# Optimization experiments

Measured on AMD Instinct MI355X. Metric: run time of the kernel, lower is better.

Reference implementation:

```python
import jax, jax.numpy as jnp
from jax import lax
import numpy as np

H = 64
IN = 32
OUT = 32


def _rnn_layer(x, Wih, Whh, bih, bhh):
    # x: [B,T,I]; PyTorch RNN: h_t = tanh(x_t Wih^T + bih + h_{t-1} Whh^T + bhh)
    B = x.shape[0]
    xW = jnp.einsum('bti,hi->bth', x, Wih) + (bih + bhh)  # fuse biases

    def step(h, xw_t):
        h_new = jnp.tanh(xw_t + h @ Whh.T)
        return h_new, h_new

    h0 = jnp.zeros((B, Whh.shape[0]), x.dtype)
    hT, outs = lax.scan(step, h0, jnp.swapaxes(xW, 0, 1))  # scan over T
    return jnp.swapaxes(outs, 0, 1), hT  # [B,T,H], [B,H]


def setup_inputs() -> dict:
    key = jax.random.key(0)
    ks = jax.random.split(key, 12)
    s1 = 1.0 / np.sqrt(H)
    u = lambda k, shape: jax.random.uniform(k, shape, jnp.float32, -s1, s1)
    return {
        'x': jax.random.normal(ks[0], (1024, 512, IN), jnp.float32),
        'Wih1': u(ks[1], (H, IN)), 'Whh1': u(ks[2], (H, H)),
        'bih1': u(ks[3], (H,)), 'bhh1': u(ks[4], (H,)),
        'Wih2': u(ks[5], (H, H)), 'Whh2': u(ks[6], (H, H)),
        'bih2': u(ks[7], (H,)), 'bhh2': u(ks[8], (H,)),
        'W_fc1': u(ks[9], (H, H)), 'b_fc1': u(ks[9], (H,)),
        'W_fc2': u(ks[10], (OUT, H)), 'b_fc2': u(ks[11], (OUT,)),
    }


def reference(x, Wih1, Whh1, bih1, bhh1, Wih2, Whh2, bih2, bhh2,
              W_fc1, b_fc1, W_fc2, b_fc2):
    out1, _ = _rnn_layer(x, Wih1, Whh1, bih1, bhh1)
    _, h2 = _rnn_layer(out1, Wih2, Whh2, bih2, bhh2)
    z = jax.nn.relu(h2 @ W_fc1.T + b_fc1)
    return z @ W_fc2.T + b_fc2  # [B,32]
```

## Files before the change

### kernel.cpp

```cpp
#include <hip/hip_runtime.h>
#include <stdint.h>

#define HH 64
#define II 32
#define TSTEPS 512
#define BATCH 1024
#define CH2 32
#define NCH2 (TSTEPS / CH2)
#define XWBYTES ((size_t)BATCH * TSTEPS * HH * 4)

typedef float f32x2 __attribute__((ext_vector_type(2)));
typedef float f32x4 __attribute__((ext_vector_type(4)));

__device__ __forceinline__ float fast_tanh(float x) {
    float e = __builtin_amdgcn_exp2f(x * 2.885390081777927f);
    return fmaf(-2.0f, __builtin_amdgcn_rcpf(e + 1.0f), 1.0f);
}

#define LOADW2(dst, src, N)                                                   \
    {                                                                         \
        const f32x4* p_ = (const f32x4*)(src);                                \
        _Pragma("unroll") for (int k_ = 0; k_ < (N) / 4; ++k_) {              \
            f32x4 v_ = p_[k_];                                                \
            dst[2 * k_] = v_.lo;                                              \
            dst[2 * k_ + 1] = v_.hi;                                          \
        }                                                                     \
    }

__global__ void __launch_bounds__(256) xw_precompute(
    const float* __restrict__ x,
    const float* __restrict__ Wih1,
    const float* __restrict__ bih1,
    const float* __restrict__ bhh1,
    float* __restrict__ xw)
{
    const int tid = threadIdx.x;
    const int w = tid >> 6;
    const int l = tid & 63;
    const int rbase = blockIdx.x * 64;

    __shared__ __align__(16) float xsm[64 * II];

    const float* gx = x + (size_t)rbase * II;
#pragma unroll
    for (int k = 0; k < 2; ++k) {
        const int off = w * 512 + k * 256;
        __builtin_amdgcn_global_load_lds(
            (const __attribute__((address_space(1))) void*)(gx + off + l * 4),
            (__attribute__((address_space(3))) void*)(xsm + off),
            16, 0, 0);
    }
    asm volatile("s_waitcnt vmcnt(0)" ::: "memory");
    __syncthreads();

    f32x2 wv[II / 2];
    LOADW2(wv, Wih1 + l * II, II);
    const float bb = bih1[l] + bhh1[l];
    float* outb = xw + (size_t)rbase * HH;

#pragma unroll
    for (int i = 0; i < 16; ++i) {
        const int r = w + i * 4;
        const float* xr = xsm + r * II;
        f32x2 a0 = {bb, 0.f}, a1 = {0.f, 0.f};
#pragma unroll
        for (int k = 0; k < II / 4; ++k) {
            f32x4 q = *(const f32x4*)(xr + 4 * k);
            a0 = __builtin_elementwise_fma(q.lo, wv[2 * k], a0);
            a1 = __builtin_elementwise_fma(q.hi, wv[2 * k + 1], a1);
        }
        outb[r * HH + l] = (a0.x + a1.x) + (a0.y + a1.y);
    }
}

__global__ void __launch_bounds__(128, 2) rnn_rec(
    const float* __restrict__ xw,
    const float* __restrict__ Whh1,
    const float* __restrict__ Wih2,
    const float* __restrict__ Whh2,
    const float* __restrict__ bih2,
    const float* __restrict__ bhh2,
    const float* __restrict__ Wfc1,
    const float* __restrict__ bfc1,
    const float* __restrict__ Wfc2,
    const float* __restrict__ bfc2,
    float* __restrict__ out)
{
    const int tid = threadIdx.x;
    const int w = tid >> 6;
    const int l = tid & 63;
    const int o = w * 32 + (l & 31);
    const int kh = l >> 5;
    const int b = blockIdx.x;

    __shared__ __align__(16) float xs[2][CH2 * HH];
    __shared__ __align__(16) float hb1[HH];
    __shared__ __align__(16) float hb2[2][HH];
    __shared__ __align__(16) float zb[HH];

    f32x2 whh1v[16], wih2v[16], whh2v[16];
    LOADW2(whh1v, Whh1 + o * HH + kh * 32, 32);
    LOADW2(wih2v, Wih2 + o * HH + kh * 32, 32);
    LOADW2(whh2v, Whh2 + o * HH + kh * 32, 32);
    const float b2 = bih2[o] + bhh2[o];

    if (tid < HH) hb2[0][tid] = 0.f;

    const float* xwb = xw + (size_t)b * TSTEPS * HH;

#pragma unroll
    for (int k = 0; k < 4; ++k) {
        const int off = (w * 4 + k) * 256;
        __builtin_amdgcn_global_load_lds(
            (const __attribute__((address_space(1))) void*)(xwb + off + l * 4),
            (__attribute__((address_space(3))) void*)(&xs[0][0] + off),
            16, 0, 0);
    }
    asm volatile("s_waitcnt vmcnt(0)" ::: "memory");
    __syncthreads();

    f32x2 h1v[16];
#pragma unroll
    for (int k = 0; k < 16; ++k) h1v[k] = f32x2{0.f, 0.f};

#define STEP(P, TT)                                                           \
    {                                                                         \
        const float xwv = cur[(TT) * HH + o];      \
        f32x2 q0 = {0.f, 0.f}, q1 = {0.f, 0.f};               \
        f32x2 r0 = {0.f, 0.f}, r1 = {0.f, 0.f};               \
        _Pragma("unroll") for (int k = 0; k < 8; ++k) {                       \
            f32x4 hq = *(const f32x4*)(&hb2[P][kh * 32 + 4 * k]);             \
            q0 = __builtin_elementwise_fma(hq.lo, whh2v[2 * k], q0);          \
            q1 = __builtin_elementwise_fma(hq.hi, whh2v[2 * k + 1], q1);      \
            r0 = __builtin_elementwise_fma(h1v[2 * k], whh1v[2 * k], r0);     \
            r1 = __builtin_elementwise_fma(h1v[2 * k + 1], whh1v[2 * k + 1], r1);\
        }                                                                     \
        const float y2c_h = (q0.x + q0.y) + (q1.x + q1.y);                    \
        float y1_h = (r0.x + r0.y) + (r1.x + r1.y);                           \
        const float y1 = y1_h + __shfl_xor(y1_h, 32);                         \
        const float h1 = fast_tanh(xwv + y1);                                 \
        if (l < 32) hb1[o] = h1;                                              \
        __syncthreads();                           \
        f32x2 s0 = {0.f, 0.f}, s1 = {0.f, 0.f};               \
        _Pragma("unroll") for (int k = 0; k < 8; ++k) {                       \
            f32x4 hq = *(const f32x4*)(&hb1[kh * 32 + 4 * k]);                \
            h1v[2 * k] = hq.lo;             \
            h1v[2 * k + 1] = hq.hi;                                           \
            s0 = __builtin_elementwise_fma(hq.lo, wih2v[2 * k], s0);          \
            s1 = __builtin_elementwise_fma(hq.hi, wih2v[2 * k + 1], s1);      \
        }                                                                     \
        float y2_h = (s0.x + s0.y) + (s1.x + s1.y) + y2c_h;                   \
        const float y2 = y2_h + __shfl_xor(y2_h, 32);                         \
        const float h2 = fast_tanh(b2 + y2);                                  \
        if (l < 32) hb2[(P) ^ 1][o] = h2;                                     \
        __syncthreads();             \
    }

#pragma unroll 1
    for (int c = 0; c < NCH2; ++c) {
        const float* cur = &xs[c & 1][0];
        float* nxt = &xs[(c & 1) ^ 1][0];
        if (c + 1 < NCH2) {
#pragma unroll
            for (int k = 0; k < 4; ++k) {
                const int off = (w * 4 + k) * 256;
                __builtin_amdgcn_global_load_lds(
                    (const __attribute__((address_space(1))) void*)(
                        xwb + (c + 1) * CH2 * HH + off + l * 4),
                    (__attribute__((address_space(3))) void*)(nxt + off),
                    16, 0, 0);
            }
        }
#pragma unroll 1
        for (int tt = 0; tt < CH2; tt += 2) {
            STEP(0, tt)
            STEP(1, tt + 1)
        }
        asm volatile("s_waitcnt vmcnt(0)" ::: "memory");
        __syncthreads();
    }

    {
        f32x2 wf[16];
        LOADW2(wf, Wfc1 + o * HH + kh * 32, 32);
        f32x2 u0 = {0.f, 0.f}, u1 = {0.f, 0.f};
#pragma unroll
        for (int k = 0; k < 8; ++k) {
            f32x4 hq = *(const f32x4*)(&hb2[0][kh * 32 + 4 * k]);
            u0 = __builtin_elementwise_fma(hq.lo, wf[2 * k], u0);
            u1 = __builtin_elementwise_fma(hq.hi, wf[2 * k + 1], u1);
        }
        float zh = (u0.x + u0.y) + (u1.x + u1.y);
        const float z = fmaxf(bfc1[o] + zh + __shfl_xor(zh, 32), 0.f);
        if (l < 32) zb[o] = z;
        __syncthreads();
    }
    {
        const int ow = w * 16 + (l & 15);
        const int kq = l >> 4;
        f32x2 wg[8];
        LOADW2(wg, Wfc2 + ow * HH + kq * 16, 16);
        f32x2 u0 = {0.f, 0.f}, u1 = {0.f, 0.f};
#pragma unroll
        for (int k = 0; k < 4; ++k) {
            f32x4 zq = *(const f32x4*)(&zb[kq * 16 + 4 * k]);
            u0 = __builtin_elementwise_fma(zq.lo, wg[2 * k], u0);
            u1 = __builtin_elementwise_fma(zq.hi, wg[2 * k + 1], u1);
        }
        float v = (u0.x + u0.y) + (u1.x + u1.y);
        v += __shfl_xor(v, 16);
        v += __shfl_xor(v, 32);
        if (l < 16) out[b * 32 + ow] = bfc2[ow] + v;
    }
}

__device__ __forceinline__ void stage8k_fb(const float* g, float* l, int lane) {
#pragma unroll
    for (int k = 0; k < 8; ++k) {
        __builtin_amdgcn_global_load_lds(
            (const __attribute__((address_space(1))) void*)(g + k * 256 + lane * 4),
            (__attribute__((address_space(3))) void*)(l + k * 256),
            16, 0, 0);
    }
}

__global__ void __launch_bounds__(256, 1) rnn_fused_fb(
    const float* __restrict__ x, const float* __restrict__ Wih1,
    const float* __restrict__ Whh1, const float* __restrict__ bih1,
    const float* __restrict__ bhh1, const float* __restrict__ Wih2,
    const float* __restrict__ Whh2, const float* __restrict__ bih2,
    const float* __restrict__ bhh2, const float* __restrict__ Wfc1,
    const float* __restrict__ bfc1, const float* __restrict__ Wfc2,
    const float* __restrict__ bfc2, float* __restrict__ out)
{
    const int wave = threadIdx.x >> 6;
    const int o = threadIdx.x & 63;
    const int b = blockIdx.x * 4 + wave;

    __shared__ __align__(16) float xs[4][2][64 * II];
    __shared__ __align__(16) float hb1[4][HH];
    __shared__ __align__(16) float hb2[4][HH];

    f32x2 wih1[II / 2], whh1[HH / 2], wih2[HH / 2], whh2[HH / 2];
    LOADW2(wih1, Wih1 + o * II, II);
    LOADW2(whh1, Whh1 + o * HH, HH);
    LOADW2(wih2, Wih2 + o * HH, HH);
    LOADW2(whh2, Whh2 + o * HH, HH);
    const float b1 = bih1[o] + bhh1[o];
    const float b2 = bih2[o] + bhh2[o];
    hb2[wave][o] = 0.f;

    const float* xb = x + (size_t)b * TSTEPS * II;
    float* l0 = &xs[wave][0][0];
    float* l1 = &xs[wave][1][0];
    stage8k_fb(xb, l0, o);
    asm volatile("s_waitcnt vmcnt(0)" ::: "memory");

    float acc1p = b1;
    float h2v = 0.f;
#pragma unroll 1
    for (int c = 0; c < TSTEPS / 64; ++c) {
        const float* cur = (c & 1) ? l1 : l0;
        float* nxt = (c & 1) ? l0 : l1;
        if (c + 1 < TSTEPS / 64) stage8k_fb(xb + (c + 1) * 64 * II, nxt, o);
#pragma unroll 1
        for (int tt = 0; tt < 64; ++tt) {
            const float* xr = cur + tt * II;
            f32x2 a0 = {acc1p, 0.f}, a1 = {0.f, 0.f};
#pragma unroll
            for (int k = 0; k < II / 4; ++k) {
                f32x4 xq = *(const f32x4*)(xr + 4 * k);
                a0 = __builtin_elementwise_fma(xq.lo, wih1[2 * k], a0);
                a1 = __builtin_elementwise_fma(xq.hi, wih1[2 * k + 1], a1);
            }
            float h1 = fast_tanh((a0.x + a1.x) + (a0.y + a1.y));
            hb1[wave][o] = h1;
            f32x2 q0 = {b2, 0.f}, q1 = {0.f, 0.f};
#pragma unroll
            for (int k = 0; k < HH / 4; ++k) {
                f32x4 hq = *(const f32x4*)(&hb2[wave][4 * k]);
                q0 = __builtin_elementwise_fma(hq.lo, whh2[2 * k], q0);
                q1 = __builtin_elementwise_fma(hq.hi, whh2[2 * k + 1], q1);
            }
            float acc2 = (q0.x + q1.x) + (q0.y + q1.y);
            f32x2 c0 = {acc2, 0.f}, c1 = {0.f, 0.f};
            f32x2 p0 = {b1, 0.f}, p1 = {0.f, 0.f};
#pragma unroll
            for (int k = 0; k < HH / 4; ++k) {
                f32x4 hq = *(const f32x4*)(&hb1[wave][4 * k]);
                c0 = __builtin_elementwise_fma(hq.lo, wih2[2 * k], c0);
                c1 = __builtin_elementwise_fma(hq.hi, wih2[2 * k + 1], c1);
                p0 = __builtin_elementwise_fma(hq.lo, whh1[2 * k], p0);
                p1 = __builtin_elementwise_fma(hq.hi, whh1[2 * k + 1], p1);
            }
            acc1p = (p0.x + p1.x) + (p0.y + p1.y);
            h2v = fast_tanh((c0.x + c1.x) + (c0.y + c1.y));
            hb2[wave][o] = h2v;
        }
        asm volatile("s_waitcnt vmcnt(0)" ::: "memory");
    }

    f32x2 wf[HH / 2];
    LOADW2(wf, Wfc1 + o * HH, HH);
    f32x2 z0 = {bfc1[o], 0.f}, z1 = {0.f, 0.f};
#pragma unroll
    for (int k = 0; k < HH / 4; ++k) {
        f32x4 hq = *(const f32x4*)(&hb2[wave][4 * k]);
        z0 = __builtin_elementwise_fma(hq.lo, wf[2 * k], z0);
        z1 = __builtin_elementwise_fma(hq.hi, wf[2 * k + 1], z1);
    }
    float z = fmaxf((z0.x + z1.x) + (z0.y + z1.y), 0.f);
    hb1[wave][o] = z;
    const int oo = o & 31;
    LOADW2(wf, Wfc2 + oo * HH, HH);
    f32x2 y0 = {bfc2[oo], 0.f}, y1 = {0.f, 0.f};
#pragma unroll
    for (int k = 0; k < HH / 4; ++k) {
        f32x4 zq = *(const f32x4*)(&hb1[wave][4 * k]);
        y0 = __builtin_elementwise_fma(zq.lo, wf[2 * k], y0);
        y1 = __builtin_elementwise_fma(zq.hi, wf[2 * k + 1], y1);
    }
    if (o < 32) out[b * 32 + oo] = (y0.x + y1.x) + (y0.y + y1.y);
}

extern "C" void kernel_launch(void* const* d_in, const int* in_sizes, int n_in,
                              void* d_out, int out_size, void* d_ws, size_t ws_size,
                              hipStream_t stream) {
    const float* x    = (const float*)d_in[0];
    const float* Wih1 = (const float*)d_in[1];
    const float* Whh1 = (const float*)d_in[2];
    const float* bih1 = (const float*)d_in[3];
    const float* bhh1 = (const float*)d_in[4];
    const float* Wih2 = (const float*)d_in[5];
    const float* Whh2 = (const float*)d_in[6];
    const float* bih2 = (const float*)d_in[7];
    const float* bhh2 = (const float*)d_in[8];
    const float* Wfc1 = (const float*)d_in[9];
    const float* bfc1 = (const float*)d_in[10];
    const float* Wfc2 = (const float*)d_in[11];
    const float* bfc2 = (const float*)d_in[12];
    float* out = (float*)d_out;

    if (ws_size >= XWBYTES) {
        float* xw = (float*)d_ws;
        hipLaunchKernelGGL(xw_precompute, dim3(BATCH * TSTEPS / 64), dim3(256),
                           0, stream, x, Wih1, bih1, bhh1, xw);
        hipLaunchKernelGGL(rnn_rec, dim3(BATCH), dim3(128), 0, stream,
                           xw, Whh1, Wih2, Whh2, bih2, bhh2,
                           Wfc1, bfc1, Wfc2, bfc2, out);
    } else {
        hipLaunchKernelGGL(rnn_fused_fb, dim3(BATCH / 4), dim3(256), 0, stream,
                           x, Wih1, Whh1, bih1, bhh1, Wih2, Whh2, bih2, bhh2,
                           Wfc1, bfc1, Wfc2, bfc2, out);
    }
}
```

Measured before the change: 462.1 us.

## Double-buffer xw precompute tiles and use raw LDS barriers in recurrence

```diff
diff --git a/kernel.cpp b/kernel.cpp
--- a/kernel.cpp
+++ b/kernel.cpp
@@ -25,6 +25,12 @@
             dst[2 * k_] = v_.lo;                                              \
             dst[2 * k_ + 1] = v_.hi;                                          \
         }                                                                     \
+    }
+
+#define LDS_BARRIER()                                                         \
+    {                                                                         \
+        asm volatile("s_waitcnt lgkmcnt(0)" ::: "memory");                    \
+        asm volatile("s_barrier" ::: "memory");                               \
     }
 
 __global__ void __launch_bounds__(256) xw_precompute(
@@ -37,39 +43,58 @@
     const int tid = threadIdx.x;
     const int w = tid >> 6;
     const int l = tid & 63;
-    const int rbase = blockIdx.x * 64;
-
-    __shared__ __align__(16) float xsm[64 * II];
-
-    const float* gx = x + (size_t)rbase * II;
-#pragma unroll
-    for (int k = 0; k < 2; ++k) {
-        const int off = w * 512 + k * 256;
-        __builtin_amdgcn_global_load_lds(
-            (const __attribute__((address_space(1))) void*)(gx + off + l * 4),
-            (__attribute__((address_space(3))) void*)(xsm + off),
-            16, 0, 0);
-    }
-    asm volatile("s_waitcnt vmcnt(0)" ::: "memory");
-    __syncthreads();
+    const int rbase = blockIdx.x * 256;
+
+    __shared__ __align__(16) float xsm[2][64 * II];
 
     f32x2 wv[II / 2];
     LOADW2(wv, Wih1 + l * II, II);
     const float bb = bih1[l] + bhh1[l];
-    float* outb = xw + (size_t)rbase * HH;
-
-#pragma unroll
-    for (int i = 0; i < 16; ++i) {
-        const int r = w + i * 4;
-        const float* xr = xsm + r * II;
-        f32x2 a0 = {bb, 0.f}, a1 = {0.f, 0.f};
-#pragma unroll
-        for (int k = 0; k < II / 4; ++k) {
-            f32x4 q = *(const f32x4*)(xr + 4 * k);
-            a0 = __builtin_elementwise_fma(q.lo, wv[2 * k], a0);
-            a1 = __builtin_elementwise_fma(q.hi, wv[2 * k + 1], a1);
-        }
-        outb[r * HH + l] = (a0.x + a1.x) + (a0.y + a1.y);
+
+    {
+        const float* gx = x + (size_t)rbase * II;
+#pragma unroll
+        for (int k = 0; k < 2; ++k) {
+            const int off = w * 512 + k * 256;
+            __builtin_amdgcn_global_load_lds(
+                (const __attribute__((address_space(1))) void*)(gx + off + l * 4),
+                (__attribute__((address_space(3))) void*)(&xsm[0][0] + off),
+                16, 0, 0);
+        }
+    }
+    asm volatile("s_waitcnt vmcnt(0)" ::: "memory");
+    asm volatile("s_barrier" ::: "memory");
+
+#pragma unroll 1
+    for (int tile = 0; tile < 4; ++tile) {
+        if (tile < 3) {
+            const float* gn = x + (size_t)(rbase + (tile + 1) * 64) * II;
+#pragma unroll
+            for (int k = 0; k < 2; ++k) {
+                const int off = w * 512 + k * 256;
+                __builtin_amdgcn_global_load_lds(
+                    (const __attribute__((address_space(1))) void*)(gn + off + l * 4),
+                    (__attribute__((address_space(3))) void*)(&xsm[(tile + 1) & 1][0] + off),
+                    16, 0, 0);
+            }
+        }
+        const float* xt = &xsm[tile & 1][0];
+        float* outb = xw + (size_t)(rbase + tile * 64) * HH;
+#pragma unroll
+        for (int i = 0; i < 16; ++i) {
+            const int r = w + i * 4;
+            const float* xr = xt + r * II;
+            f32x2 a0 = {bb, 0.f}, a1 = {0.f, 0.f};
+#pragma unroll
+            for (int k = 0; k < II / 4; ++k) {
+                f32x4 q = *(const f32x4*)(xr + 4 * k);
+                a0 = __builtin_elementwise_fma(q.lo, wv[2 * k], a0);
+                a1 = __builtin_elementwise_fma(q.hi, wv[2 * k + 1], a1);
+            }
+            outb[r * HH + l] = (a0.x + a1.x) + (a0.y + a1.y);
+        }
+        asm volatile("s_waitcnt vmcnt(0)" ::: "memory");
+        asm volatile("s_barrier" ::: "memory");
     }
 }
 
@@ -116,8 +141,8 @@
             (__attribute__((address_space(3))) void*)(&xs[0][0] + off),
             16, 0, 0);
     }
-    asm volatile("s_waitcnt vmcnt(0)" ::: "memory");
-    __syncthreads();
+    asm volatile("s_waitcnt vmcnt(0) lgkmcnt(0)" ::: "memory");
+    asm volatile("s_barrier" ::: "memory");
 
     f32x2 h1v[16];
 #pragma unroll
@@ -125,7 +150,7 @@
 
 #define STEP(P, TT)                                                           \
     {                                                                         \
-        const float xwv = cur[(TT) * HH + o];      \
+        const float xwv = cur[(TT) * HH + o];       \
         f32x2 q0 = {0.f, 0.f}, q1 = {0.f, 0.f};               \
         f32x2 r0 = {0.f, 0.f}, r1 = {0.f, 0.f};               \
         _Pragma("unroll") for (int k = 0; k < 8; ++k) {                       \
@@ -140,7 +165,7 @@
         const float y1 = y1_h + __shfl_xor(y1_h, 32);                         \
         const float h1 = fast_tanh(xwv + y1);                                 \
         if (l < 32) hb1[o] = h1;                                              \
-        __syncthreads();                           \
+        LDS_BARRIER()                                         \
         f32x2 s0 = {0.f, 0.f}, s1 = {0.f, 0.f};               \
         _Pragma("unroll") for (int k = 0; k < 8; ++k) {                       \
             f32x4 hq = *(const f32x4*)(&hb1[kh * 32 + 4 * k]);                \
@@ -153,7 +178,7 @@
         const float y2 = y2_h + __shfl_xor(y2_h, 32);                         \
         const float h2 = fast_tanh(b2 + y2);                                  \
         if (l < 32) hb2[(P) ^ 1][o] = h2;                                     \
-        __syncthreads();             \
+        LDS_BARRIER()                           \
     }
 
 #pragma unroll 1
@@ -177,7 +202,7 @@
             STEP(1, tt + 1)
         }
         asm volatile("s_waitcnt vmcnt(0)" ::: "memory");
-        __syncthreads();
+        asm volatile("s_barrier" ::: "memory");
     }
 
     {
@@ -343,7 +368,7 @@
 
     if (ws_size >= XWBYTES) {
         float* xw = (float*)d_ws;
-        hipLaunchKernelGGL(xw_precompute, dim3(BATCH * TSTEPS / 64), dim3(256),
+        hipLaunchKernelGGL(xw_precompute, dim3(BATCH * TSTEPS / 256), dim3(256),
                            0, stream, x, Wih1, bih1, bhh1, xw);
         hipLaunchKernelGGL(rnn_rec, dim3(BATCH), dim3(128), 0, stream,
                            xw, Whh1, Wih2, Whh2, bih2, bhh2,
```

Result: no change. 462.9 us (+0.2%).
